# Kernel tuning notes

Hardware: AMD Instinct MI355X
Metric: run time of the kernel (lower is better)

## Reference

```python
import jax, jax.numpy as jnp
import numpy as np

LAYERS, STACKS = 10, 4
DILATIONS = [2 ** l for _ in range(STACKS) for l in range(LAYERS)]  # 40 blocks


def setup_inputs() -> dict:
    key = jax.random.key(0)
    ks = jax.random.split(key, 7)
    B, C, L, SC, NB = 4, 64, 8192, 256, len(DILATIONS)
    scale = 0.05  # keep 40 stacked residual blocks numerically tame
    return {
        "x": jax.random.normal(ks[0], (B, C, L), dtype=jnp.float32),
        "dc_w": jax.random.normal(ks[1], (NB, C, C, 2), dtype=jnp.float32) * scale,
        "dc_b": jax.random.normal(ks[2], (NB, C), dtype=jnp.float32) * scale,
        "conv_w": jax.random.normal(ks[3], (NB, C, C), dtype=jnp.float32) * scale,
        "conv_b": jax.random.normal(ks[4], (NB, C), dtype=jnp.float32) * scale,
        "skip_w": jax.random.normal(ks[5], (NB, SC, C), dtype=jnp.float32) * scale,
        "skip_b": jax.random.normal(ks[6], (NB, SC), dtype=jnp.float32) * scale,
        "skip_size": 4096,
    }


def reference(x, dc_w, dc_b, conv_w, conv_b, skip_w, skip_b, skip_size):
    # x: [B, res_ch, L]; returns stacked skips [n_blocks, B, skip_ch, skip_size]
    out = x
    skips = []
    for i, d in enumerate(DILATIONS):
        h = (jnp.einsum('oi,bil->bol', dc_w[i, :, :, 0], out[:, :, :-d])
             + jnp.einsum('oi,bil->bol', dc_w[i, :, :, 1], out[:, :, d:])
             + dc_b[i][None, :, None])
        g = jax.nn.relu(h)
        r = jnp.einsum('oi,bil->bol', conv_w[i], g) + conv_b[i][None, :, None]
        out = r + out[:, :, -r.shape[2]:]  # residual on aligned (last) timesteps
        s = jnp.einsum('oi,bil->bol', skip_w[i], g) + skip_b[i][None, :, None]
        skips.append(s[:, :, -skip_size:])
    return jnp.stack(skips)
```

## Files before the change

### kernel.cpp

```cpp
#include <hip/hip_runtime.h>


#define CC    64
#define SCC   256
#define BB    4
#define LL0   8192
#define NBLK  40
#define SKIPN 4096

typedef __attribute__((ext_vector_type(8))) short bf16x8;
typedef __attribute__((ext_vector_type(4))) float f32x4;
typedef unsigned short us;

__device__ __forceinline__ us f2bf(float f) {
    union { float f; unsigned u; } v; v.f = f;
    return (us)((v.u + 0x7FFF + ((v.u >> 16) & 1)) >> 16);
}
__device__ __forceinline__ unsigned pk2(float a, float b) {
    return (unsigned)f2bf(a) | ((unsigned)f2bf(b) << 16);
}
__device__ __forceinline__ uint2 pk4(f32x4 v) {
    return (uint2){pk2(v[0], v[1]), pk2(v[2], v[3])};
}
__device__ __forceinline__ bf16x8 pack8(f32x4 u0, f32x4 u1) {
    bf16x8 r;
    r[0]=(short)f2bf(u0[0]); r[1]=(short)f2bf(u0[1]);
    r[2]=(short)f2bf(u0[2]); r[3]=(short)f2bf(u0[3]);
    r[4]=(short)f2bf(u1[0]); r[5]=(short)f2bf(u1[1]);
    r[6]=(short)f2bf(u1[2]); r[7]=(short)f2bf(u1[3]);
    return r;
}
__device__ __forceinline__ int sws(int r, int c) {
    return (r << 6) + ((((c >> 3) ^ r) & 7) << 3) + (c & 7);
}
__device__ __forceinline__ int scb(int s, int chunk) {
    return (s << 6) + (((chunk ^ (s & 7)) & 7) << 3);
}

__global__ __launch_bounds__(256) void prep_kernel(
    const float* __restrict__ x, float* __restrict__ xt_out,
    const float* __restrict__ dc_w, const float* __restrict__ conv_w,
    const float* __restrict__ skip_w,
    us* __restrict__ wcat, us* __restrict__ cwb, us* __restrict__ swb)
{
    if (blockIdx.x < 512) {
        __shared__ float tile[64][65];
        const int b = blockIdx.x >> 7, t0 = (blockIdx.x & 127) * 64;
        const int tid = threadIdx.x;
        #pragma unroll
        for (int p = 0; p < 4; ++p) {
            const int c = p * 16 + (tid >> 4), j = tid & 15;
            const float4 v = *(const float4*)(x + ((size_t)b * CC + c) * LL0 + t0 + j * 4);
            tile[c][j*4+0]=v.x; tile[c][j*4+1]=v.y; tile[c][j*4+2]=v.z; tile[c][j*4+3]=v.w;
        }
        __syncthreads();
        #pragma unroll
        for (int p = 0; p < 4; ++p) {
            const int r = p * 16 + (tid >> 4), h = tid & 15;
            float4 v = {tile[h*4+0][r], tile[h*4+1][r], tile[h*4+2][r], tile[h*4+3][r]};
            *(float4*)(xt_out + ((size_t)b * LL0 + t0 + r) * CC + h * 4) = v;
        }
        return;
    }
    const int n_sw = NBLK * SCC * CC, n_cw = NBLK * CC * CC, n_wc = NBLK * CC * 128;
    for (int idx = (blockIdx.x - 512) * blockDim.x + threadIdx.x; idx < n_sw;
         idx += 1024 * blockDim.x) {
        swb[idx] = f2bf(skip_w[idx]);
        if (idx < n_cw) cwb[idx] = f2bf(conv_w[idx]);
        if (idx < n_wc) {
            const int i = idx >> 13, o = (idx >> 7) & 63, kk = idx & 127;
            wcat[idx] = f2bf(dc_w[(((i * CC + o) * CC) + (kk & 63)) * 2 + (kk >> 6)]);
        }
    }
}

template<int NW>
__device__ __forceinline__ void skip_body(
    int e, int blk0,
    const us* __restrict__ g_all, const us* __restrict__ swb,
    const float* __restrict__ skip_b, float* __restrict__ out)
{
    constexpr int ROWS = NW * 16;
    constexpr int TPB = (SKIPN / ROWS) * BB;
    const int tid = threadIdx.x, lane = tid & 63, wv = tid >> 6;
    const int j = blk0 + e / TPB;
    const int id = e % TPB;
    const int tt = id % (SKIPN / ROWS);
    const int b  = id / (SKIPN / ROWS);
    const us* g  = g_all + ((size_t)j * BB + b) * SKIPN * CC;
    const us* sw = swb + (size_t)j * SCC * CC;
    const float* sb = skip_b + j * SCC;
    float* op = out + ((size_t)j * BB + b) * SCC * SKIPN;

    const int trow = tt * ROWS + wv * 16 + (lane & 15);
    bf16x8 a[2];
    a[0] = *(const bf16x8*)(g + (size_t)trow * CC + (lane >> 4) * 8);
    a[1] = *(const bf16x8*)(g + (size_t)trow * CC + 32 + (lane >> 4) * 8);
    const int tstore = tt * ROWS + wv * 16 + ((lane >> 4) << 2);
    #pragma unroll 4
    for (int n = 0; n < 16; ++n) {
        const int sc = n * 16 + (lane & 15);
        const float bias = sb[sc];
        f32x4 acc = (f32x4){bias, bias, bias, bias};
        const us* wrow = sw + sc * CC + (lane >> 4) * 8;
        acc = __builtin_amdgcn_mfma_f32_16x16x32_bf16(a[0], *(const bf16x8*)(wrow), acc, 0, 0, 0);
        acc = __builtin_amdgcn_mfma_f32_16x16x32_bf16(a[1], *(const bf16x8*)(wrow + 32), acc, 0, 0, 0);
        *(float4*)(op + (size_t)sc * SKIPN + tstore) = (float4){acc[0], acc[1], acc[2], acc[3]};
    }
}

__global__ __launch_bounds__(512) void fused6_kernel(
    const float* __restrict__ cur, float* __restrict__ nxt,
    const us* __restrict__ wcat_all, const us* __restrict__ cwb_all,
    const float* __restrict__ db_all, const float* __restrict__ cb_all,
    us* __restrict__ g_all, int blk0, int Lin, int ntiles,
    const us* __restrict__ swb, const float* __restrict__ skip_b,
    float* __restrict__ out, int pb0)
{
    const int wg = blockIdx.x, chain = BB * ntiles;
    if (wg >= chain) { skip_body<8>(wg - chain, pb0, g_all, swb, skip_b, out); return; }

    constexpr int TOUT = 96, R0 = 159, RCAP = 160;
    __shared__ __align__(16) float sm[RCAP * CC];
    __shared__ __align__(16) us  scr[8 * 16 * CC];

    const int tid = threadIdx.x, lane = tid & 63, wv = tid >> 6;
    const int b = wg / ntiles, t0 = (wg % ntiles) * TOUT;
    const float* src = cur + (size_t)b * LL0 * CC;
    const int s = lane & 15, q = lane >> 4;
    us* myscr = scr + wv * (16 * CC);

    for (int base = 0; base < R0; base += 32) {
        const int row = base + (tid >> 4);
        const int h4 = (tid & 15) * 4;
        if (row < R0) {
            int gt = t0 + row; if (gt > Lin - 1) gt = Lin - 1;
            *(f32x4*)(sm + sws(row, h4)) = *(const f32x4*)(src + (size_t)gt * CC + h4);
        }
    }
    __syncthreads();

    int Rcur = R0, Lj = Lin;
    for (int j = 0; j < 6; ++j) {
        const int d = 1 << j;
        const int Rn = Rcur - d;
        Lj -= d;
        const us* wj = wcat_all + (size_t)(blk0 + j) * CC * 128;
        const us* cj = cwb_all + (size_t)(blk0 + j) * CC * CC;
        const float* dbj = db_all + (blk0 + j) * CC;
        const float* cbj = cb_all + (blk0 + j) * CC;
        const int wbase = Lj - SKIPN;
        us* gdst = g_all + ((size_t)(blk0 + j) * BB + b) * SKIPN * CC;

        f32x4 r2[2][4];
        #pragma unroll
        for (int fi = 0; fi < 2; ++fi) {
            const int fg = wv + fi * 8;
            const bool act = fg * 16 < Rn;
            if (act) {
                const int t = fg * 16 + s;
                const int tc = t > Rn - 1 ? Rn - 1 : t;
                bf16x8 af0 = pack8(*(const f32x4*)(sm + sws(tc, q * 8)),
                                   *(const f32x4*)(sm + sws(tc, q * 8 + 4)));
                bf16x8 af1 = pack8(*(const f32x4*)(sm + sws(tc, 32 + q * 8)),
                                   *(const f32x4*)(sm + sws(tc, 36 + q * 8)));
                bf16x8 af2 = pack8(*(const f32x4*)(sm + sws(tc + d, q * 8)),
                                   *(const f32x4*)(sm + sws(tc + d, q * 8 + 4)));
                bf16x8 af3 = pack8(*(const f32x4*)(sm + sws(tc + d, 32 + q * 8)),
                                   *(const f32x4*)(sm + sws(tc + d, 36 + q * 8)));
                #pragma unroll
                for (int n = 0; n < 4; ++n) {
                    const int o0 = n * 16 + q * 4;
                    f32x4 acc = *(const f32x4*)(dbj + o0);
                    const us* wr = wj + (n * 16 + s) * 128 + q * 8;
                    acc = __builtin_amdgcn_mfma_f32_16x16x32_bf16(*(const bf16x8*)(wr),      af0, acc, 0, 0, 0);
                    acc = __builtin_amdgcn_mfma_f32_16x16x32_bf16(*(const bf16x8*)(wr + 32), af1, acc, 0, 0, 0);
                    acc = __builtin_amdgcn_mfma_f32_16x16x32_bf16(*(const bf16x8*)(wr + 64), af2, acc, 0, 0, 0);
                    acc = __builtin_amdgcn_mfma_f32_16x16x32_bf16(*(const bf16x8*)(wr + 96), af3, acc, 0, 0, 0);
                    #pragma unroll
                    for (int r = 0; r < 4; ++r) acc[r] = acc[r] > 0.f ? acc[r] : 0.f;
                    *(uint2*)(myscr + scb(s, n * 2 + (q >> 1)) + (q & 1) * 4) = pk4(acc);
                }
                {
                    const int gt = t0 + t;
                    if (t < Rn && gt >= wbase && gt < Lj) {
                        us* gr = gdst + (size_t)(gt - wbase) * CC;
                        #pragma unroll
                        for (int h = 0; h < 2; ++h) {
                            const int ck = q * 2 + h;
                            *(bf16x8*)(gr + ck * 8) = *(const bf16x8*)(myscr + scb(s, ck));
                        }
                    }
                }
                bf16x8 g0 = *(const bf16x8*)(myscr + scb(s, q));
                bf16x8 g1 = *(const bf16x8*)(myscr + scb(s, 4 + q));
                #pragma unroll
                for (int n = 0; n < 4; ++n) {
                    const int o0 = n * 16 + q * 4;
                    f32x4 r = *(const f32x4*)(cbj + o0);
                    const us* wr = cj + (n * 16 + s) * CC + q * 8;
                    r = __builtin_amdgcn_mfma_f32_16x16x32_bf16(*(const bf16x8*)(wr),      g0, r, 0, 0, 0);
                    r = __builtin_amdgcn_mfma_f32_16x16x32_bf16(*(const bf16x8*)(wr + 32), g1, r, 0, 0, 0);
                    r += *(const f32x4*)(sm + sws(tc + d, o0));
                    r2[fi][n] = r;
                }
            }
        }
        __syncthreads();
        #pragma unroll
        for (int fi = 0; fi < 2; ++fi) {
            const int fg = wv + fi * 8;
            const int t = fg * 16 + s;
            if (t < Rn) {
                #pragma unroll
                for (int n = 0; n < 4; ++n)
                    *(f32x4*)(sm + sws(t, n * 16 + q * 4)) = r2[fi][n];
            }
        }
        __syncthreads();
        Rcur = Rn;
    }

    float* dst = nxt + (size_t)b * LL0 * CC;
    for (int base = 0; base < TOUT; base += 32) {
        const int row = base + (tid >> 4);
        const int h4 = (tid & 15) * 4;
        const int gt = t0 + row;
        if (row < TOUT && gt < Lj)
            *(float4*)(dst + (size_t)gt * CC + h4) = *(const float4*)(sm + sws(row, h4));
    }
}

template<int D>
__global__ __launch_bounds__(256) void pair_kernel(
    const float* __restrict__ cur, float* __restrict__ nxt,
    const us* __restrict__ wA, const us* __restrict__ wB,
    const us* __restrict__ cA, const us* __restrict__ cB,
    const float* __restrict__ dbA, const float* __restrict__ dbB,
    const float* __restrict__ cbA, const float* __restrict__ cbB,
    us* __restrict__ gA_out, us* __restrict__ gB_out,
    int Lin, int ntB,
    const us* __restrict__ g_all, const us* __restrict__ swb,
    const float* __restrict__ skip_b, float* __restrict__ out, int pb0)
{
    const int wg = blockIdx.x, chain = BB * ntB;
    if (wg >= chain) { skip_body<4>(wg - chain, pb0, g_all, swb, skip_b, out); return; }

    __shared__ __align__(16) float xs[4 * 32 * CC];
    __shared__ __align__(16) float ms[2 * 32 * CC];
    __shared__ __align__(16) us  scr[4 * 16 * CC];

    const int tid = threadIdx.x, lane = tid & 63, wv = tid >> 6;
    const int b = wg / ntB, T0 = (wg % ntB) * 32;
    const float* src = cur + (size_t)b * LL0 * CC;
    const int s = lane & 15, q = lane >> 4;
    us* myscr = scr + wv * (16 * CC);
    const int LoutA = Lin - D, Lout2 = Lin - 3 * D;

    #pragma unroll
    for (int p = 0; p < 8; ++p) {
        const int row = p * 16 + (tid >> 4);
        const int st = row >> 5, r = row & 31;
        const int h4 = (tid & 15) * 4;
        int gt = T0 + st * D + r; if (gt > Lin - 1) gt = Lin - 1;
        *(f32x4*)(xs + st * (32 * CC) + sws(r, h4)) =
            *(const f32x4*)(src + (size_t)gt * CC + h4);
    }
    __syncthreads();

    {
        const int m = wv >> 1, rA = (wv & 1) * 16 + s;
        const int tA = T0 + m * 2 * D + rA;
        const float* x0 = xs + (2 * m) * (32 * CC);
        const float* x1 = xs + (2 * m + 1) * (32 * CC);
        bf16x8 af0 = pack8(*(const f32x4*)(x0 + sws(rA, q * 8)),
                           *(const f32x4*)(x0 + sws(rA, q * 8 + 4)));
        bf16x8 af1 = pack8(*(const f32x4*)(x0 + sws(rA, 32 + q * 8)),
                           *(const f32x4*)(x0 + sws(rA, 36 + q * 8)));
        bf16x8 af2 = pack8(*(const f32x4*)(x1 + sws(rA, q * 8)),
                           *(const f32x4*)(x1 + sws(rA, q * 8 + 4)));
        bf16x8 af3 = pack8(*(const f32x4*)(x1 + sws(rA, 32 + q * 8)),
                           *(const f32x4*)(x1 + sws(rA, 36 + q * 8)));
        #pragma unroll
        for (int n = 0; n < 4; ++n) {
            const int o0 = n * 16 + q * 4;
            f32x4 acc = *(const f32x4*)(dbA + o0);
            const us* wr = wA + (n * 16 + s) * 128 + q * 8;
            acc = __builtin_amdgcn_mfma_f32_16x16x32_bf16(*(const bf16x8*)(wr),      af0, acc, 0, 0, 0);
            acc = __builtin_amdgcn_mfma_f32_16x16x32_bf16(*(const bf16x8*)(wr + 32), af1, acc, 0, 0, 0);
            acc = __builtin_amdgcn_mfma_f32_16x16x32_bf16(*(const bf16x8*)(wr + 64), af2, acc, 0, 0, 0);
            acc = __builtin_amdgcn_mfma_f32_16x16x32_bf16(*(const bf16x8*)(wr + 96), af3, acc, 0, 0, 0);
            #pragma unroll
            for (int r = 0; r < 4; ++r) acc[r] = acc[r] > 0.f ? acc[r] : 0.f;
            *(uint2*)(myscr + scb(s, n * 2 + (q >> 1)) + (q & 1) * 4) = pk4(acc);
        }
        {
            const int wbA = LoutA - SKIPN;
            const bool own = (m == 0) || (tA >= ntB * 32);
            if (own && tA >= wbA && tA < LoutA) {
                us* gr = gA_out + ((size_t)b * SKIPN + (tA - wbA)) * CC;
                #pragma unroll
                for (int h = 0; h < 2; ++h) {
                    const int ck = q * 2 + h;
                    *(bf16x8*)(gr + ck * 8) = *(const bf16x8*)(myscr + scb(s, ck));
                }
            }
        }
        bf16x8 g0 = *(const bf16x8*)(myscr + scb(s, q));
        bf16x8 g1 = *(const bf16x8*)(myscr + scb(s, 4 + q));
        #pragma unroll
        for (int n = 0; n < 4; ++n) {
            const int o0 = n * 16 + q * 4;
            f32x4 r = *(const f32x4*)(cbA + o0);
            const us* wr = cA + (n * 16 + s) * CC + q * 8;
            r = __builtin_amdgcn_mfma_f32_16x16x32_bf16(*(const bf16x8*)(wr),      g0, r, 0, 0, 0);
            r = __builtin_amdgcn_mfma_f32_16x16x32_bf16(*(const bf16x8*)(wr + 32), g1, r, 0, 0, 0);
            r += *(const f32x4*)(x1 + sws(rA, o0));
            *(f32x4*)(ms + m * (32 * CC) + sws(rA, o0)) = r;
        }
    }
    __syncthreads();

    {
        const int rB = (wv & 1) * 16 + s;
        const int tB = T0 + rB;
        const bool lead = wv < 2;
        const float* m0 = ms;
        const float* m1 = ms + 32 * CC;
        bf16x8 af0 = pack8(*(const f32x4*)(m0 + sws(rB, q * 8)),
                           *(const f32x4*)(m0 + sws(rB, q * 8 + 4)));
        bf16x8 af1 = pack8(*(const f32x4*)(m0 + sws(rB, 32 + q * 8)),
                           *(const f32x4*)(m0 + sws(rB, 36 + q * 8)));
        bf16x8 af2 = pack8(*(const f32x4*)(m1 + sws(rB, q * 8)),
                           *(const f32x4*)(m1 + sws(rB, q * 8 + 4)));
        bf16x8 af3 = pack8(*(const f32x4*)(m1 + sws(rB, 32 + q * 8)),
                           *(const f32x4*)(m1 + sws(rB, 36 + q * 8)));
        #pragma unroll
        for (int n = 0; n < 4; ++n) {
            const int o0 = n * 16 + q * 4;
            f32x4 acc = *(const f32x4*)(dbB + o0);
            const us* wr = wB + (n * 16 + s) * 128 + q * 8;
            acc = __builtin_amdgcn_mfma_f32_16x16x32_bf16(*(const bf16x8*)(wr),      af0, acc, 0, 0, 0);
            acc = __builtin_amdgcn_mfma_f32_16x16x32_bf16(*(const bf16x8*)(wr + 32), af1, acc, 0, 0, 0);
            acc = __builtin_amdgcn_mfma_f32_16x16x32_bf16(*(const bf16x8*)(wr + 64), af2, acc, 0, 0, 0);
            acc = __builtin_amdgcn_mfma_f32_16x16x32_bf16(*(const bf16x8*)(wr + 96), af3, acc, 0, 0, 0);
            #pragma unroll
            for (int r = 0; r < 4; ++r) acc[r] = acc[r] > 0.f ? acc[r] : 0.f;
            *(uint2*)(myscr + scb(s, n * 2 + (q >> 1)) + (q & 1) * 4) = pk4(acc);
        }
        {
            const int wbB = Lout2 - SKIPN;
            if (lead && tB >= wbB && tB < Lout2) {
                us* gr = gB_out + ((size_t)b * SKIPN + (tB - wbB)) * CC;
                #pragma unroll
                for (int h = 0; h < 2; ++h) {
                    const int ck = q * 2 + h;
                    *(bf16x8*)(gr + ck * 8) = *(const bf16x8*)(myscr + scb(s, ck));
                }
            }
        }
        bf16x8 g0 = *(const bf16x8*)(myscr + scb(s, q));
        bf16x8 g1 = *(const bf16x8*)(myscr + scb(s, 4 + q));
        float* dst = nxt + (size_t)b * LL0 * CC;
        #pragma unroll
        for (int n = 0; n < 4; ++n) {
            const int o0 = n * 16 + q * 4;
            f32x4 r = *(const f32x4*)(cbB + o0);
            const us* wr = cB + (n * 16 + s) * CC + q * 8;
            r = __builtin_amdgcn_mfma_f32_16x16x32_bf16(*(const bf16x8*)(wr),      g0, r, 0, 0, 0);
            r = __builtin_amdgcn_mfma_f32_16x16x32_bf16(*(const bf16x8*)(wr + 32), g1, r, 0, 0, 0);
            r += *(const f32x4*)(m1 + sws(rB, o0));
            if (lead && tB < Lout2)
                *(f32x4*)(dst + (size_t)tB * CC + o0) = r;
        }
    }
}

__global__ __launch_bounds__(256) void skip_kernel(
    const us* __restrict__ g_all, const us* __restrict__ swb,
    const float* __restrict__ skip_b, float* __restrict__ out, int blk0)
{
    skip_body<4>(blockIdx.x, blk0, g_all, swb, skip_b, out);
}

extern "C" void kernel_launch(void* const* d_in, const int* in_sizes, int n_in,
                              void* d_out, int out_size, void* d_ws, size_t ws_size,
                              hipStream_t stream)
{
    const float* x      = (const float*)d_in[0];
    const float* dc_w   = (const float*)d_in[1];
    const float* dc_b   = (const float*)d_in[2];
    const float* conv_w = (const float*)d_in[3];
    const float* conv_b = (const float*)d_in[4];
    const float* skip_w = (const float*)d_in[5];
    const float* skip_b = (const float*)d_in[6];
    float* out = (float*)d_out;

    char* ws = (char*)d_ws;
    float* bufA = (float*)ws;  ws += (size_t)BB * LL0 * CC * 4;
    float* bufB = (float*)ws;  ws += (size_t)BB * LL0 * CC * 4;
    us* g_all = (us*)ws;       ws += (size_t)NBLK * BB * SKIPN * CC * 2;
    us* wcat  = (us*)ws;       ws += (size_t)NBLK * CC * 128 * 2;
    us* cwb   = (us*)ws;       ws += (size_t)NBLK * CC * CC * 2;
    us* swb   = (us*)ws;       ws += (size_t)NBLK * SCC * CC * 2;

    prep_kernel<<<1536, 256, 0, stream>>>(x, bufA, dc_w, conv_w, skip_w, wcat, cwb, swb);

    float* bufs[2] = {bufA, bufB};
    const size_t GSZ = (size_t)BB * SKIPN * CC;
    int Lc = LL0, blk = 0, q = 0, produced = 0, skipped = 0;
    for (int st = 0; st < 4; ++st) {
        {
            const int Lout = Lc - 63;
            const int nt = (Lout + 95) / 96;
            int cap = produced - skipped; if (cap > 4) cap = 4;
            fused6_kernel<<<dim3(BB * nt + cap * 128), 512, 0, stream>>>(
                bufs[q & 1], bufs[(q + 1) & 1], wcat, cwb, dc_b, conv_b,
                g_all, blk, Lc, nt, swb, skip_b, out, skipped);
            skipped += cap; produced += 6; blk += 6; Lc = Lout; ++q;
        }
        #pragma unroll
        for (int pi = 0; pi < 2; ++pi) {
            const int D = pi == 0 ? 64 : 256;
            const int Lout2 = Lc - 3 * D;
            const int nt = (Lout2 + 31) / 32;
            int cap = produced - skipped; if (cap > 4) cap = 4;
            const int grid = BB * nt + cap * 256;
            if (D == 64)
                pair_kernel<64><<<dim3(grid), 256, 0, stream>>>(
                    bufs[q & 1], bufs[(q + 1) & 1],
                    wcat + (size_t)blk * CC * 128, wcat + (size_t)(blk + 1) * CC * 128,
                    cwb + (size_t)blk * CC * CC, cwb + (size_t)(blk + 1) * CC * CC,
                    dc_b + blk * CC, dc_b + (blk + 1) * CC,
                    conv_b + blk * CC, conv_b + (blk + 1) * CC,
                    g_all + (size_t)blk * GSZ, g_all + (size_t)(blk + 1) * GSZ,
                    Lc, nt, g_all, swb, skip_b, out, skipped);
            else
                pair_kernel<256><<<dim3(grid), 256, 0, stream>>>(
                    bufs[q & 1], bufs[(q + 1) & 1],
                    wcat + (size_t)blk * CC * 128, wcat + (size_t)(blk + 1) * CC * 128,
                    cwb + (size_t)blk * CC * CC, cwb + (size_t)(blk + 1) * CC * CC,
                    dc_b + blk * CC, dc_b + (blk + 1) * CC,
                    conv_b + blk * CC, conv_b + (blk + 1) * CC,
                    g_all + (size_t)blk * GSZ, g_all + (size_t)(blk + 1) * GSZ,
                    Lc, nt, g_all, swb, skip_b, out, skipped);
            skipped += cap; produced += 2; blk += 2; Lc = Lout2; ++q;
        }
    }
    const int rem = NBLK - skipped;
    if (rem > 0)
        skip_kernel<<<dim3(rem * 256), 256, 0, stream>>>(g_all, swb, skip_b, out, skipped);
}
```

Before: 770.5 us.

## Replace pair kernels with single-layer kernels and keep bf16 activation copies in LDS

Each dilation 64..512 layer now runs in its own single_kernel with 64-row tiles and 512 threads, replacing the two-layer pair_kernel that recomputed intermediate rows. The fused6 kernel and single_kernel keep a bf16 copy of activations in shared memory, so MFMA operands are loaded directly instead of packed from fp32 on every read. The skip GEMM moves to 8-wave blocks everywhere. This adds kernel launches and an extra global round-trip per layer in exchange for less redundant compute and less conversion work, and the extra LDS buffer may lower occupancy in fused6.

```diff
diff --git a/kernel.cpp b/kernel.cpp
--- a/kernel.cpp
+++ b/kernel.cpp
@@ -22,15 +22,10 @@
 __device__ __forceinline__ uint2 pk4(f32x4 v) {
     return (uint2){pk2(v[0], v[1]), pk2(v[2], v[3])};
 }
-__device__ __forceinline__ bf16x8 pack8(f32x4 u0, f32x4 u1) {
-    bf16x8 r;
-    r[0]=(short)f2bf(u0[0]); r[1]=(short)f2bf(u0[1]);
-    r[2]=(short)f2bf(u0[2]); r[3]=(short)f2bf(u0[3]);
-    r[4]=(short)f2bf(u1[0]); r[5]=(short)f2bf(u1[1]);
-    r[6]=(short)f2bf(u1[2]); r[7]=(short)f2bf(u1[3]);
-    return r;
-}
 __device__ __forceinline__ int sws(int r, int c) {
+    return (r << 6) + ((((c >> 3) ^ r) & 7) << 3) + (c & 7);
+}
+__device__ __forceinline__ int swh(int r, int c) {
     return (r << 6) + ((((c >> 3) ^ r) & 7) << 3) + (c & 7);
 }
 __device__ __forceinline__ int scb(int s, int chunk) {
@@ -74,13 +69,12 @@
     }
 }
 
-template<int NW>
-__device__ __forceinline__ void skip_body(
+__device__ __forceinline__ void skip_body8(
     int e, int blk0,
     const us* __restrict__ g_all, const us* __restrict__ swb,
     const float* __restrict__ skip_b, float* __restrict__ out)
 {
-    constexpr int ROWS = NW * 16;
+    constexpr int ROWS = 128;
     constexpr int TPB = (SKIPN / ROWS) * BB;
     const int tid = threadIdx.x, lane = tid & 63, wv = tid >> 6;
     const int j = blk0 + e / TPB;
@@ -118,10 +112,11 @@
     float* __restrict__ out, int pb0)
 {
     const int wg = blockIdx.x, chain = BB * ntiles;
-    if (wg >= chain) { skip_body<8>(wg - chain, pb0, g_all, swb, skip_b, out); return; }
+    if (wg >= chain) { skip_body8(wg - chain, pb0, g_all, swb, skip_b, out); return; }
 
     constexpr int TOUT = 96, R0 = 159, RCAP = 160;
     __shared__ __align__(16) float sm[RCAP * CC];
+    __shared__ __align__(16) us  smb[RCAP * CC];
     __shared__ __align__(16) us  scr[8 * 16 * CC];
 
     const int tid = threadIdx.x, lane = tid & 63, wv = tid >> 6;
@@ -135,7 +130,9 @@
         const int h4 = (tid & 15) * 4;
         if (row < R0) {
             int gt = t0 + row; if (gt > Lin - 1) gt = Lin - 1;
-            *(f32x4*)(sm + sws(row, h4)) = *(const f32x4*)(src + (size_t)gt * CC + h4);
+            f32x4 v = *(const f32x4*)(src + (size_t)gt * CC + h4);
+            *(f32x4*)(sm + sws(row, h4)) = v;
+            *(uint2*)(smb + swh(row, h4)) = pk4(v);
         }
     }
     __syncthreads();
@@ -156,18 +153,13 @@
         #pragma unroll
         for (int fi = 0; fi < 2; ++fi) {
             const int fg = wv + fi * 8;
-            const bool act = fg * 16 < Rn;
-            if (act) {
+            if (fg * 16 < Rn) {
                 const int t = fg * 16 + s;
                 const int tc = t > Rn - 1 ? Rn - 1 : t;
-                bf16x8 af0 = pack8(*(const f32x4*)(sm + sws(tc, q * 8)),
-                                   *(const f32x4*)(sm + sws(tc, q * 8 + 4)));
-                bf16x8 af1 = pack8(*(const f32x4*)(sm + sws(tc, 32 + q * 8)),
-                                   *(const f32x4*)(sm + sws(tc, 36 + q * 8)));
-                bf16x8 af2 = pack8(*(const f32x4*)(sm + sws(tc + d, q * 8)),
-                                   *(const f32x4*)(sm + sws(tc + d, q * 8 + 4)));
-                bf16x8 af3 = pack8(*(const f32x4*)(sm + sws(tc + d, 32 + q * 8)),
-                                   *(const f32x4*)(sm + sws(tc + d, 36 + q * 8)));
+                bf16x8 af0 = *(const bf16x8*)(smb + swh(tc,     q * 8));
+                bf16x8 af1 = *(const bf16x8*)(smb + swh(tc,     32 + q * 8));
+                bf16x8 af2 = *(const bf16x8*)(smb + swh(tc + d, q * 8));
+                bf16x8 af3 = *(const bf16x8*)(smb + swh(tc + d, 32 + q * 8));
                 #pragma unroll
                 for (int n = 0; n < 4; ++n) {
                     const int o0 = n * 16 + q * 4;
@@ -181,6 +173,8 @@
                     for (int r = 0; r < 4; ++r) acc[r] = acc[r] > 0.f ? acc[r] : 0.f;
                     *(uint2*)(myscr + scb(s, n * 2 + (q >> 1)) + (q & 1) * 4) = pk4(acc);
                 }
+                bf16x8 g0 = *(const bf16x8*)(myscr + scb(s, q));
+                bf16x8 g1 = *(const bf16x8*)(myscr + scb(s, 4 + q));
                 {
                     const int gt = t0 + t;
                     if (t < Rn && gt >= wbase && gt < Lj) {
@@ -192,8 +186,6 @@
                         }
                     }
                 }
-                bf16x8 g0 = *(const bf16x8*)(myscr + scb(s, q));
-                bf16x8 g1 = *(const bf16x8*)(myscr + scb(s, 4 + q));
                 #pragma unroll
                 for (int n = 0; n < 4; ++n) {
                     const int o0 = n * 16 + q * 4;
@@ -213,8 +205,11 @@
             const int t = fg * 16 + s;
             if (t < Rn) {
                 #pragma unroll
-                for (int n = 0; n < 4; ++n)
-                    *(f32x4*)(sm + sws(t, n * 16 + q * 4)) = r2[fi][n];
+                for (int n = 0; n < 4; ++n) {
+                    const int o0 = n * 16 + q * 4;
+                    *(f32x4*)(sm + sws(t, o0)) = r2[fi][n];
+                    *(uint2*)(smb + swh(t, o0)) = pk4(r2[fi][n]);
+                }
             }
         }
         __syncthreads();
@@ -231,156 +226,95 @@
     }
 }
 
-template<int D>
-__global__ __launch_bounds__(256) void pair_kernel(
+__global__ __launch_bounds__(512) void single_kernel(
     const float* __restrict__ cur, float* __restrict__ nxt,
-    const us* __restrict__ wA, const us* __restrict__ wB,
-    const us* __restrict__ cA, const us* __restrict__ cB,
-    const float* __restrict__ dbA, const float* __restrict__ dbB,
-    const float* __restrict__ cbA, const float* __restrict__ cbB,
-    us* __restrict__ gA_out, us* __restrict__ gB_out,
-    int Lin, int ntB,
+    const us* __restrict__ wcat, const us* __restrict__ cwb,
+    const float* __restrict__ db, const float* __restrict__ cb,
+    us* __restrict__ g_out,
+    int d, int Lin, int Lout, int ntiles,
     const us* __restrict__ g_all, const us* __restrict__ swb,
     const float* __restrict__ skip_b, float* __restrict__ out, int pb0)
 {
-    const int wg = blockIdx.x, chain = BB * ntB;
-    if (wg >= chain) { skip_body<4>(wg - chain, pb0, g_all, swb, skip_b, out); return; }
-
-    __shared__ __align__(16) float xs[4 * 32 * CC];
-    __shared__ __align__(16) float ms[2 * 32 * CC];
-    __shared__ __align__(16) us  scr[4 * 16 * CC];
+    const int wg = blockIdx.x, chain = BB * ntiles;
+    if (wg >= chain) { skip_body8(wg - chain, pb0, g_all, swb, skip_b, out); return; }
+
+    __shared__ __align__(16) us   xb0[64 * CC];
+    __shared__ __align__(16) us   xb1[64 * CC];
+    __shared__ __align__(16) float x1f[64 * CC];
+    __shared__ __align__(16) us   scr[8 * 16 * CC];
 
     const int tid = threadIdx.x, lane = tid & 63, wv = tid >> 6;
-    const int b = wg / ntB, T0 = (wg % ntB) * 32;
+    const int b = wg / ntiles, t0 = (wg % ntiles) * 64;
     const float* src = cur + (size_t)b * LL0 * CC;
     const int s = lane & 15, q = lane >> 4;
     us* myscr = scr + wv * (16 * CC);
-    const int LoutA = Lin - D, Lout2 = Lin - 3 * D;
+    const int Lv = (Lout - t0) < 64 ? (Lout - t0) : 64;
 
     #pragma unroll
-    for (int p = 0; p < 8; ++p) {
-        const int row = p * 16 + (tid >> 4);
-        const int st = row >> 5, r = row & 31;
+    for (int p = 0; p < 2; ++p) {
+        const int row = p * 32 + (tid >> 4);
         const int h4 = (tid & 15) * 4;
-        int gt = T0 + st * D + r; if (gt > Lin - 1) gt = Lin - 1;
-        *(f32x4*)(xs + st * (32 * CC) + sws(r, h4)) =
-            *(const f32x4*)(src + (size_t)gt * CC + h4);
+        int ta = t0 + row;     if (ta > Lin - 1) ta = Lin - 1;
+        int tb = t0 + row + d; if (tb > Lin - 1) tb = Lin - 1;
+        f32x4 v0 = *(const f32x4*)(src + (size_t)ta * CC + h4);
+        f32x4 v1 = *(const f32x4*)(src + (size_t)tb * CC + h4);
+        *(uint2*)(xb0 + swh(row, h4)) = pk4(v0);
+        *(uint2*)(xb1 + swh(row, h4)) = pk4(v1);
+        *(f32x4*)(x1f + sws(row, h4)) = v1;
     }
     __syncthreads();
 
+    const int tl = wv * 16 + s;
+    const int tc = tl > Lv - 1 ? Lv - 1 : tl;
+    bf16x8 af0 = *(const bf16x8*)(xb0 + swh(tc, q * 8));
+    bf16x8 af1 = *(const bf16x8*)(xb0 + swh(tc, 32 + q * 8));
+    bf16x8 af2 = *(const bf16x8*)(xb1 + swh(tc, q * 8));
+    bf16x8 af3 = *(const bf16x8*)(xb1 + swh(tc, 32 + q * 8));
+    #pragma unroll
+    for (int n = 0; n < 4; ++n) {
+        const int o0 = n * 16 + q * 4;
+        f32x4 acc = *(const f32x4*)(db + o0);
+        const us* wr = wcat + (n * 16 + s) * 128 + q * 8;
+        acc = __builtin_amdgcn_mfma_f32_16x16x32_bf16(*(const bf16x8*)(wr),      af0, acc, 0, 0, 0);
+        acc = __builtin_amdgcn_mfma_f32_16x16x32_bf16(*(const bf16x8*)(wr + 32), af1, acc, 0, 0, 0);
+        acc = __builtin_amdgcn_mfma_f32_16x16x32_bf16(*(const bf16x8*)(wr + 64), af2, acc, 0, 0, 0);
+        acc = __builtin_amdgcn_mfma_f32_16x16x32_bf16(*(const bf16x8*)(wr + 96), af3, acc, 0, 0, 0);
+        #pragma unroll
+        for (int r = 0; r < 4; ++r) acc[r] = acc[r] > 0.f ? acc[r] : 0.f;
+        *(uint2*)(myscr + scb(s, n * 2 + (q >> 1)) + (q & 1) * 4) = pk4(acc);
+    }
+    bf16x8 g0 = *(const bf16x8*)(myscr + scb(s, q));
+    bf16x8 g1 = *(const bf16x8*)(myscr + scb(s, 4 + q));
     {
-        const int m = wv >> 1, rA = (wv & 1) * 16 + s;
-        const int tA = T0 + m * 2 * D + rA;
-        const float* x0 = xs + (2 * m) * (32 * CC);
-        const float* x1 = xs + (2 * m + 1) * (32 * CC);
-        bf16x8 af0 = pack8(*(const f32x4*)(x0 + sws(rA, q * 8)),
-                           *(const f32x4*)(x0 + sws(rA, q * 8 + 4)));
-        bf16x8 af1 = pack8(*(const f32x4*)(x0 + sws(rA, 32 + q * 8)),
-                           *(const f32x4*)(x0 + sws(rA, 36 + q * 8)));
-        bf16x8 af2 = pack8(*(const f32x4*)(x1 + sws(rA, q * 8)),
-                           *(const f32x4*)(x1 + sws(rA, q * 8 + 4)));
-        bf16x8 af3 = pack8(*(const f32x4*)(x1 + sws(rA, 32 + q * 8)),
-                           *(const f32x4*)(x1 + sws(rA, 36 + q * 8)));
-        #pragma unroll
-        for (int n = 0; n < 4; ++n) {
-            const int o0 = n * 16 + q * 4;
-            f32x4 acc = *(const f32x4*)(dbA + o0);
-            const us* wr = wA + (n * 16 + s) * 128 + q * 8;
-            acc = __builtin_amdgcn_mfma_f32_16x16x32_bf16(*(const bf16x8*)(wr),      af0, acc, 0, 0, 0);
-            acc = __builtin_amdgcn_mfma_f32_16x16x32_bf16(*(const bf16x8*)(wr + 32), af1, acc, 0, 0, 0);
-            acc = __builtin_amdgcn_mfma_f32_16x16x32_bf16(*(const bf16x8*)(wr + 64), af2, acc, 0, 0, 0);
-            acc = __builtin_amdgcn_mfma_f32_16x16x32_bf16(*(const bf16x8*)(wr + 96), af3, acc, 0, 0, 0);
+        const int gt = t0 + tl;
+        const int wb = Lout - SKIPN;
+        if (tl < Lv && gt >= wb) {
+            us* gr = g_out + ((size_t)b * SKIPN + (gt - wb)) * CC;
             #pragma unroll
-            for (int r = 0; r < 4; ++r) acc[r] = acc[r] > 0.f ? acc[r] : 0.f;
-            *(uint2*)(myscr + scb(s, n * 2 + (q >> 1)) + (q & 1) * 4) = pk4(acc);
-        }
-        {
-            const int wbA = LoutA - SKIPN;
-            const bool own = (m == 0) || (tA >= ntB * 32);
-            if (own && tA >= wbA && tA < LoutA) {
-                us* gr = gA_out + ((size_t)b * SKIPN + (tA - wbA)) * CC;
-                #pragma unroll
-                for (int h = 0; h < 2; ++h) {
-                    const int ck = q * 2 + h;
-                    *(bf16x8*)(gr + ck * 8) = *(const bf16x8*)(myscr + scb(s, ck));
-                }
+            for (int h = 0; h < 2; ++h) {
+                const int ck = q * 2 + h;
+                *(bf16x8*)(gr + ck * 8) = *(const bf16x8*)(myscr + scb(s, ck));
             }
         }
-        bf16x8 g0 = *(const bf16x8*)(myscr + scb(s, q));
-        bf16x8 g1 = *(const bf16x8*)(myscr + scb(s, 4 + q));
-        #pragma unroll
-        for (int n = 0; n < 4; ++n) {
-            const int o0 = n * 16 + q * 4;
-            f32x4 r = *(const f32x4*)(cbA + o0);
-            const us* wr = cA + (n * 16 + s) * CC + q * 8;
-            r = __builtin_amdgcn_mfma_f32_16x16x32_bf16(*(const bf16x8*)(wr),      g0, r, 0, 0, 0);
-            r = __builtin_amdgcn_mfma_f32_16x16x32_bf16(*(const bf16x8*)(wr + 32), g1, r, 0, 0, 0);
-            r += *(const f32x4*)(x1 + sws(rA, o0));
-            *(f32x4*)(ms + m * (32 * CC) + sws(rA, o0)) = r;
-        }
-    }
-    __syncthreads();
-
-    {
-        const int rB = (wv & 1) * 16 + s;
-        const int tB = T0 + rB;
-        const bool lead = wv < 2;
-        const float* m0 = ms;
-        const float* m1 = ms + 32 * CC;
-        bf16x8 af0 = pack8(*(const f32x4*)(m0 + sws(rB, q * 8)),
-                           *(const f32x4*)(m0 + sws(rB, q * 8 + 4)));
-        bf16x8 af1 = pack8(*(const f32x4*)(m0 + sws(rB, 32 + q * 8)),
-                           *(const f32x4*)(m0 + sws(rB, 36 + q * 8)));
-        bf16x8 af2 = pack8(*(const f32x4*)(m1 + sws(rB, q * 8)),
-                           *(const f32x4*)(m1 + sws(rB, q * 8 + 4)));
-        bf16x8 af3 = pack8(*(const f32x4*)(m1 + sws(rB, 32 + q * 8)),
-                           *(const f32x4*)(m1 + sws(rB, 36 + q * 8)));
-        #pragma unroll
-        for (int n = 0; n < 4; ++n) {
-            const int o0 = n * 16 + q * 4;
-            f32x4 acc = *(const f32x4*)(dbB + o0);
-            const us* wr = wB + (n * 16 + s) * 128 + q * 8;
-            acc = __builtin_amdgcn_mfma_f32_16x16x32_bf16(*(const bf16x8*)(wr),      af0, acc, 0, 0, 0);
-            acc = __builtin_amdgcn_mfma_f32_16x16x32_bf16(*(const bf16x8*)(wr + 32), af1, acc, 0, 0, 0);
-            acc = __builtin_amdgcn_mfma_f32_16x16x32_bf16(*(const bf16x8*)(wr + 64), af2, acc, 0, 0, 0);
-            acc = __builtin_amdgcn_mfma_f32_16x16x32_bf16(*(const bf16x8*)(wr + 96), af3, acc, 0, 0, 0);
-            #pragma unroll
-            for (int r = 0; r < 4; ++r) acc[r] = acc[r] > 0.f ? acc[r] : 0.f;
-            *(uint2*)(myscr + scb(s, n * 2 + (q >> 1)) + (q & 1) * 4) = pk4(acc);
-        }
-        {
-            const int wbB = Lout2 - SKIPN;
-            if (lead && tB >= wbB && tB < Lout2) {
-                us* gr = gB_out + ((size_t)b * SKIPN + (tB - wbB)) * CC;
-                #pragma unroll
-                for (int h = 0; h < 2; ++h) {
-                    const int ck = q * 2 + h;
-                    *(bf16x8*)(gr + ck * 8) = *(const bf16x8*)(myscr + scb(s, ck));
-                }
-            }
-        }
-        bf16x8 g0 = *(const bf16x8*)(myscr + scb(s, q));
-        bf16x8 g1 = *(const bf16x8*)(myscr + scb(s, 4 + q));
-        float* dst = nxt + (size_t)b * LL0 * CC;
-        #pragma unroll
-        for (int n = 0; n < 4; ++n) {
-            const int o0 = n * 16 + q * 4;
-            f32x4 r = *(const f32x4*)(cbB + o0);
-            const us* wr = cB + (n * 16 + s) * CC + q * 8;
-            r = __builtin_amdgcn_mfma_f32_16x16x32_bf16(*(const bf16x8*)(wr),      g0, r, 0, 0, 0);
-            r = __builtin_amdgcn_mfma_f32_16x16x32_bf16(*(const bf16x8*)(wr + 32), g1, r, 0, 0, 0);
-            r += *(const f32x4*)(m1 + sws(rB, o0));
-            if (lead && tB < Lout2)
-                *(f32x4*)(dst + (size_t)tB * CC + o0) = r;
-        }
-    }
-}
-
-__global__ __launch_bounds__(256) void skip_kernel(
+    }
+    float* dst = nxt + (size_t)b * LL0 * CC + (size_t)(t0 + tl) * CC;
+    #pragma unroll
+    for (int n = 0; n < 4; ++n) {
+        const int o0 = n * 16 + q * 4;
+        f32x4 r = *(const f32x4*)(cb + o0);
+        const us* wr = cwb + (n * 16 + s) * CC + q * 8;
+        r = __builtin_amdgcn_mfma_f32_16x16x32_bf16(*(const bf16x8*)(wr),      g0, r, 0, 0, 0);
+        r = __builtin_amdgcn_mfma_f32_16x16x32_bf16(*(const bf16x8*)(wr + 32), g1, r, 0, 0, 0);
+        r += *(const f32x4*)(x1f + sws(tl < 63 ? tl : 63, o0));
+        if (tl < Lv) *(f32x4*)(dst + o0) = r;
+    }
+}
+
+__global__ __launch_bounds__(512) void skip_kernel(
     const us* __restrict__ g_all, const us* __restrict__ swb,
     const float* __restrict__ skip_b, float* __restrict__ out, int blk0)
 {
-    skip_body<4>(blockIdx.x, blk0, g_all, swb, skip_b, out);
+    skip_body8(blockIdx.x, blk0, g_all, swb, skip_b, out);
 }
 
 extern "C" void kernel_launch(void* const* d_in, const int* in_sizes, int n_in,
@@ -400,54 +334,40 @@
     float* bufA = (float*)ws;  ws += (size_t)BB * LL0 * CC * 4;
     float* bufB = (float*)ws;  ws += (size_t)BB * LL0 * CC * 4;
     us* g_all = (us*)ws;       ws += (size_t)NBLK * BB * SKIPN * CC * 2;
-    us* wcat  = (us*)ws;       ws += (size_t)NBLK * CC * 128 * 2;
-    us* cwb   = (us*)ws;       ws += (size_t)NBLK * CC * CC * 2;
-    us* swb   = (us*)ws;       ws += (size_t)NBLK * SCC * CC * 2;
+    us* wcat = (us*)ws;        ws += (size_t)NBLK * CC * 128 * 2;
+    us* cwb  = (us*)ws;        ws += (size_t)NBLK * CC * CC * 2;
+    us* swb  = (us*)ws;        ws += (size_t)NBLK * SCC * CC * 2;
 
     prep_kernel<<<1536, 256, 0, stream>>>(x, bufA, dc_w, conv_w, skip_w, wcat, cwb, swb);
 
     float* bufs[2] = {bufA, bufB};
     const size_t GSZ = (size_t)BB * SKIPN * CC;
-    int Lc = LL0, blk = 0, q = 0, produced = 0, skipped = 0;
+    int Lc = LL0, blk = 0, qq = 0, produced = 0, skipped = 0;
     for (int st = 0; st < 4; ++st) {
         {
             const int Lout = Lc - 63;
             const int nt = (Lout + 95) / 96;
             int cap = produced - skipped; if (cap > 4) cap = 4;
             fused6_kernel<<<dim3(BB * nt + cap * 128), 512, 0, stream>>>(
-                bufs[q & 1], bufs[(q + 1) & 1], wcat, cwb, dc_b, conv_b,
+                bufs[qq & 1], bufs[(qq + 1) & 1], wcat, cwb, dc_b, conv_b,
                 g_all, blk, Lc, nt, swb, skip_b, out, skipped);
-            skipped += cap; produced += 6; blk += 6; Lc = Lout; ++q;
-        }
-        #pragma unroll
-        for (int pi = 0; pi < 2; ++pi) {
-            const int D = pi == 0 ? 64 : 256;
-            const int Lout2 = Lc - 3 * D;
-            const int nt = (Lout2 + 31) / 32;
+            skipped += cap; produced += 6; blk += 6; Lc = Lout; ++qq;
+        }
+        for (int dl = 6; dl < 10; ++dl) {
+            const int d = 1 << dl;
+            const int Lout = Lc - d;
+            const int nt = (Lout + 63) / 64;
             int cap = produced - skipped; if (cap > 4) cap = 4;
-            const int grid = BB * nt + cap * 256;
-            if (D == 64)
-                pair_kernel<64><<<dim3(grid), 256, 0, stream>>>(
-                    bufs[q & 1], bufs[(q + 1) & 1],
-                    wcat + (size_t)blk * CC * 128, wcat + (size_t)(blk + 1) * CC * 128,
-                    cwb + (size_t)blk * CC * CC, cwb + (size_t)(blk + 1) * CC * CC,
-                    dc_b + blk * CC, dc_b + (blk + 1) * CC,
-                    conv_b + blk * CC, conv_b + (blk + 1) * CC,
-                    g_all + (size_t)blk * GSZ, g_all + (size_t)(blk + 1) * GSZ,
-                    Lc, nt, g_all, swb, skip_b, out, skipped);
-            else
-                pair_kernel<256><<<dim3(grid), 256, 0, stream>>>(
-                    bufs[q & 1], bufs[(q + 1) & 1],
-                    wcat + (size_t)blk * CC * 128, wcat + (size_t)(blk + 1) * CC * 128,
-                    cwb + (size_t)blk * CC * CC, cwb + (size_t)(blk + 1) * CC * CC,
-                    dc_b + blk * CC, dc_b + (blk + 1) * CC,
-                    conv_b + blk * CC, conv_b + (blk + 1) * CC,
-                    g_all + (size_t)blk * GSZ, g_all + (size_t)(blk + 1) * GSZ,
-                    Lc, nt, g_all, swb, skip_b, out, skipped);
-            skipped += cap; produced += 2; blk += 2; Lc = Lout2; ++q;
+            single_kernel<<<dim3(BB * nt + cap * 128), 512, 0, stream>>>(
+                bufs[qq & 1], bufs[(qq + 1) & 1],
+                wcat + (size_t)blk * CC * 128, cwb + (size_t)blk * CC * CC,
+                dc_b + blk * CC, conv_b + blk * CC,
+                g_all + (size_t)blk * GSZ,
+                d, Lc, Lout, nt, g_all, swb, skip_b, out, skipped);
+            skipped += cap; produced += 1; blk += 1; Lc = Lout; ++qq;
         }
     }
     const int rem = NBLK - skipped;
     if (rem > 0)
-        skip_kernel<<<dim3(rem * 256), 256, 0, stream>>>(g_all, swb, skip_b, out, skipped);
-}
+        skip_kernel<<<dim3(rem * 128), 512, 0, stream>>>(g_all, swb, skip_b, out, skipped);
+}
```

Result: slower. 854.0 us (+10.8%).
